# Performance work log

Measured on AMD Instinct MI355X. Metric: run time of the kernel, lower is better.

## Reference

```python
import jax, jax.numpy as jnp
import numpy as np

EPS = 1e-5
DELTA = 0.2
VIS_LAM = 1.0


def setup_inputs() -> dict:
    key = jax.random.key(0)
    k1, k2, k3 = jax.random.split(key, 3)
    Na, Ns, Nb, Ne, D = 16, 32, 100, 12, 512
    vis_feats = jax.random.normal(k1, (Na * Ns * Nb, D), dtype=jnp.float32)
    word_feats = jax.random.normal(k2, (Na * Ne, D), dtype=jnp.float32)
    entities_length = jax.random.randint(k3, (Na,), 0, Ne).astype(jnp.int64)
    return {"vis_feats": vis_feats, "word_feats": word_feats,
            "entities_length": entities_length, "Nb": Nb}


def reference(vis_feats, word_feats, entities_length, Nb):
    Na = entities_length.shape[0]
    Ne = word_feats.shape[0] // Na
    Ns = vis_feats.shape[0] // (Na * Nb)
    D = vis_feats.shape[1]
    ent = entities_length

    div_vec = jnp.where(ent == 0, 1, ent).astype(vis_feats.dtype)      # (Na,)
    # pad mask: entity slot e is padding for action a if e >= ent[a]
    col_mask = jnp.arange(Ne)[None, :] >= ent[:, None]                 # (Na, Ne)

    # masked similarity: (Na*Ns*Nb, Na*Ne)
    S_ = vis_feats @ word_feats.T
    S_ = jnp.where(col_mask.reshape(-1)[None, :], 0.0, S_)

    # --- train-only visual consistency loss ---
    S_vt = S_.reshape(Na, Ns, Nb, Na, Ne)
    # diagonal over the two action axes: S_vis[i] = S_vt[i,:,:,i,:]
    S_vis = S_vt[jnp.arange(Na), :, :, jnp.arange(Na), :]              # (Na, Ns, Nb, Ne)
    S_vis_ng = jax.lax.stop_gradient(S_vis)                            # torch.no_grad block
    sim_scr = S_vis_ng.max(axis=2)                                     # (Na, Ns, Ne)
    maxind = jnp.argmax(S_vis_ng, axis=2)                              # (Na, Ns, Ne)
    smin = sim_scr.min(axis=1, keepdims=True)
    smax = sim_scr.max(axis=1, keepdims=True)
    sim_scr = ((sim_scr - smin) / (smax - smin + EPS))[..., None]      # (Na, Ns, Ne, 1)

    # NOTE: original code indexes vis_feats with the raw box index (< Nb);
    # reproduced faithfully.
    vcls = vis_feats[maxind.reshape(-1)].reshape(Na, Ns, Ne, D)
    vcls = vcls / (jnp.linalg.norm(vcls, axis=3, keepdims=True) + EPS)
    vcls = vcls * sim_scr
    v1 = vcls.transpose(0, 2, 1, 3)                                    # (Na, Ne, Ns, D)
    vis_mat = 1.0 - jnp.einsum('aesd,aetd->aest', v1, v1)              # (Na, Ne, Ns, Ns)
    eye = jnp.eye(Ns, dtype=bool)
    mvis = col_mask[:, :, None, None] | eye[None, None, :, :]
    vis_mat = jnp.where(mvis, 0.0, vis_mat)
    dem = jnp.count_nonzero(vis_mat).astype(vis_mat.dtype)
    vis_loss = vis_mat.sum() / dem

    # --- margin loss over frame-level scores ---
    S = S_.reshape(Na * Ns, Nb, Na * Ne).max(axis=1).reshape(Na, Ns, Na * Ne)
    Smin = S.min(axis=1, keepdims=True)
    Smax = S.max(axis=1, keepdims=True)
    S = S * ((S - Smin) / (Smax - Smin + EPS))
    Sf = S.reshape(Na, Ns, Na, Ne).sum(-1) / div_vec                   # (Na, Ns, Na)
    Sf_diag = Sf[jnp.arange(Na), :, jnp.arange(Na)]                    # (Na, Ns)
    term1 = jax.nn.relu(Sf - Sf_diag.T[None, :, :] + DELTA).mean(0).T  # (Na, Ns)
    term2 = jax.nn.relu(Sf - Sf_diag[:, :, None] + DELTA).mean(2)      # (Na, Ns)
    frame_score = term1 + term2
    margin_loss = (frame_score.mean() + VIS_LAM * vis_loss) * 10.0

    S_sim = S_.reshape(Na * Ns, Nb, Na * Ne)
    D_sim = S_sim.max(axis=1)
    D_ind = jnp.argmax(S_sim, axis=1)
    return (D_ind, D_sim, margin_loss)
```

## Files before the change

kernel.cpp:

```cpp
#include <hip/hip_runtime.h>
#include <math.h>

#define NA 16
#define NS 32
#define NB 100
#define NE 12
#define DD 512
#define NQ (NA*NS)
#define NC (NA*NE)
#define OUT_SIM_OFF (NQ*NC)
#define EPSF 1e-5f
#define DELTAF 0.2f
#define EPS_R 0.15f

#define WS_B_FOFF 12288

typedef _Float16 f16x8 __attribute__((ext_vector_type(8)));
typedef float f32x4 __attribute__((ext_vector_type(4)));

__global__ __launch_bounds__(64) void k0_conv(
    const float* __restrict__ word, float* __restrict__ ws)
{
    const int kcc = blockIdx.x / 12;
    const int nt  = blockIdx.x - kcc*12;
    const int l   = threadIdx.x;
    if (blockIdx.x == 0 && l < 2) ws[l] = 0.f;

    const int col = nt*16 + (l & 15);
    const int k   = kcc*32 + (l >> 4)*8;
    const float* src = word + (size_t)col*DD + k;
    float4 v0 = *(const float4*)(src);
    float4 v1 = *(const float4*)(src + 4);
    f16x8 hv;
    hv[0]=(_Float16)v0.x; hv[1]=(_Float16)v0.y; hv[2]=(_Float16)v0.z; hv[3]=(_Float16)v0.w;
    hv[4]=(_Float16)v1.x; hv[5]=(_Float16)v1.y; hv[6]=(_Float16)v1.z; hv[7]=(_Float16)v1.w;
    unsigned short* wsB = (unsigned short*)(ws + WS_B_FOFF);
    *(f16x8*)&wsB[(size_t)kcc*6144 + nt*512 + l*8] = hv;
}

__global__ __launch_bounds__(512, 4) void k1_mfma(
    const float* __restrict__ vis, const float* __restrict__ word,
    const unsigned short* __restrict__ wsB,
    const int* __restrict__ ent, float* __restrict__ out)
{
    __shared__ __align__(16) char pool[40960];
    unsigned short* Abuf = (unsigned short*)pool;
    unsigned short* Bbuf = (unsigned short*)(pool + 16384);
    float* part_v = (float*)pool;
    int*   part_i = (int*)(pool + 1536);
    float* colmax = (float*)(pool + 3072);
    int*   cnts   = (int*)(pool + 3840);
    int*   cand   = (int*)(pool + 4608);
    int*   flist  = (int*)(pool + 5376);
    int*   nflag  = (int*)(pool + 6144);

    const int t    = threadIdx.x;
    const int lane = t & 63;
    const int wid  = t >> 6;
    const int wm   = wid >> 2;
    const int wn   = wid & 3;
    const int q    = blockIdx.x;
    const float* visq = vis + (size_t)q * NB * DD;

    f32x4 acc[4][3];
    #pragma unroll
    for (int mi = 0; mi < 4; mi++)
        #pragma unroll
        for (int ni = 0; ni < 3; ni++) acc[mi][ni] = (f32x4)0.f;

    #define A_LOAD(av0, av1, kb)                                               \
        {   int l_ = t & 63;                                                   \
            int row = ((t >> 6) << 4) + (l_ & 15);                             \
            av0 = make_float4(0.f,0.f,0.f,0.f);                                \
            av1 = make_float4(0.f,0.f,0.f,0.f);                                \
            if (row < NB) {                                                    \
                const float* p_ = visq + (size_t)row*DD + (kb) + ((l_>>4)<<3); \
                av0 = *(const float4*)p_;                                      \
                av1 = *(const float4*)(p_ + 4); } }
    #define A_STORE(av0, av1, pn)                                              \
        {   f16x8 hv;                                                          \
            hv[0]=(_Float16)av0.x; hv[1]=(_Float16)av0.y;                      \
            hv[2]=(_Float16)av0.z; hv[3]=(_Float16)av0.w;                      \
            hv[4]=(_Float16)av1.x; hv[5]=(_Float16)av1.y;                      \
            hv[6]=(_Float16)av1.z; hv[7]=(_Float16)av1.w;                      \
            *(f16x8*)&Abuf[(pn)*4096 + t*8] = hv; }
    #define B_STAGE(kcn, pn)                                                   \
        {   const unsigned short* bsrc = wsB + (size_t)(kcn)*6144;             \
            unsigned short* bdst = Bbuf + (pn)*6144;                           \
            __builtin_amdgcn_global_load_lds(                                  \
                (const void*)(bsrc + ((size_t)(wid*64 + lane))*8),             \
                (void*)(bdst + (wid*64)*8), 16, 0, 0);                         \
            if (wid < 4)                                                       \
                __builtin_amdgcn_global_load_lds(                              \
                    (const void*)(bsrc + ((size_t)(512 + wid*64 + lane))*8),   \
                    (void*)(bdst + (512 + wid*64)*8), 16, 0, 0); }

    {
        B_STAGE(0, 0);
        float4 a0, a1;
        A_LOAD(a0, a1, 0);
        A_STORE(a0, a1, 0);
    }
    __syncthreads();

    for (int kc = 0; kc < 16; ++kc) {
        const int p = kc & 1;
        float4 a0, a1;
        if (kc < 15) {
            A_LOAD(a0, a1, (kc+1)*32);
            B_STAGE(kc+1, p^1);
        }
        {
            const unsigned short* Bp = Bbuf + p*6144;
            const unsigned short* Ap = Abuf + p*4096;
            f16x8 bf[3];
            #pragma unroll
            for (int ni = 0; ni < 3; ni++)
                bf[ni] = *((const f16x8*)&Bp[(wn*3 + ni)*512 + lane*8]);
            #pragma unroll
            for (int mi = 0; mi < 4; mi++) {
                f16x8 af = *((const f16x8*)&Ap[(wm*4 + mi)*512 + lane*8]);
                #pragma unroll
                for (int ni = 0; ni < 3; ni++)
                    acc[mi][ni] = __builtin_amdgcn_mfma_f32_16x16x32_f16(af, bf[ni], acc[mi][ni], 0, 0, 0);
            }
        }
        if (kc < 15) { A_STORE(a0, a1, (p^1)); }
        __syncthreads();
    }

    #pragma unroll
    for (int ni = 0; ni < 3; ni++) {
        float bv = -INFINITY; int bg = 1000;
        #pragma unroll
        for (int mi = 0; mi < 4; mi++)
            #pragma unroll
            for (int r = 0; r < 4; r++) {
                int g = wm*64 + mi*16 + ((lane>>4)<<2) + r;
                float v = acc[mi][ni][r];
                if (g < NB && (v > bv || (v == bv && g < bg))) { bv = v; bg = g; }
            }
        #pragma unroll
        for (int off = 16; off <= 32; off <<= 1) {
            float ov = __shfl_xor(bv, off);
            int   og = __shfl_xor(bg, off);
            if (ov > bv || (ov == bv && og < bg)) { bv = ov; bg = og; }
        }
        if (lane < 16) {
            int col = wn*48 + ni*16 + lane;
            part_v[wm*NC + col] = bv; part_i[wm*NC + col] = bg;
        }
    }
    if (t < NC) { cnts[t] = 0; cand[t] = 0; }
    if (t == 0) *nflag = 0;
    __syncthreads();

    float fbv = 0.f; int fbg = 0; bool fmask = true;
    if (t < NC) {
        fbv = part_v[t]; fbg = part_i[t];
        float v1 = part_v[NC + t]; int g1 = part_i[NC + t];
        if (v1 > fbv || (v1 == fbv && g1 < fbg)) { fbv = v1; fbg = g1; }
        int a2 = t / NE, e = t - a2*NE;
        fmask = (e >= ent[a2]);
        colmax[t] = fmask ? INFINITY : fbv;
    }
    __syncthreads();

    #pragma unroll
    for (int ni = 0; ni < 3; ni++) {
        int col = wn*48 + ni*16 + (lane & 15);
        float cm = colmax[col] - EPS_R;
        #pragma unroll
        for (int mi = 0; mi < 4; mi++)
            #pragma unroll
            for (int r = 0; r < 4; r++) {
                int g = wm*64 + mi*16 + ((lane>>4)<<2) + r;
                float v = acc[mi][ni][r];
                if (g < NB && v >= cm) {
                    int s = atomicAdd(&cnts[col], 1);
                    if (s < 3) atomicOr(&cand[col], (g + 1) << (8*s));
                }
            }
    }
    __syncthreads();

    if (t < NC) {
        if (fmask) {
            out[(size_t)q*NC + t] = 0.f;
            out[OUT_SIM_OFF + (size_t)q*NC + t] = 0.f;
        } else if (cnts[t] <= 1) {
            out[(size_t)q*NC + t] = (float)fbg;
            out[OUT_SIM_OFF + (size_t)q*NC + t] = fbv;
        } else {
            int idx = atomicAdd(nflag, 1);
            flist[idx] = t;
        }
    }
    __syncthreads();

    const int nf = *nflag;
    for (int f = wid; f < nf; f += 8) {
        int col = flist[f];
        int cnt = cnts[col];
        const float* wc = word + (size_t)col*DD;
        float bv; int bg;
        if (cnt <= 3) {
            int grp = lane >> 4, li = lane & 15;
            int cpk = cand[col];
            int myrow = (grp < cnt) ? (((cpk >> (8*grp)) & 255) - 1) : -1;
            float d = 0.f;
            if (myrow >= 0) {
                const float* vr = visq + (size_t)myrow*DD + li*32;
                const float* wb = wc + li*32;
                #pragma unroll
                for (int m = 0; m < 8; ++m) {
                    float4 a = *(const float4*)(vr + m*4);
                    float4 b = *(const float4*)(wb + m*4);
                    d = fmaf(a.x, b.x, d); d = fmaf(a.y, b.y, d);
                    d = fmaf(a.z, b.z, d); d = fmaf(a.w, b.w, d);
                }
            }
            #pragma unroll
            for (int off = 1; off <= 8; off <<= 1) d += __shfl_xor(d, off);
            float v0 = __shfl(d, 0), v1 = __shfl(d, 16), v2 = __shfl(d, 32);
            int r0 = ( cpk        & 255) - 1;
            int r1 = ((cpk >> 8)  & 255) - 1;
            int r2 = ((cpk >> 16) & 255) - 1;
            bv = v0; bg = r0;
            if (cnt >= 2 && (v1 > bv || (v1 == bv && r1 < bg))) { bv = v1; bg = r1; }
            if (cnt >= 3 && (v2 > bv || (v2 == bv && r2 < bg))) { bv = v2; bg = r2; }
        } else {
            float mbv = -INFINITY; int mbg = 1000;
            for (int r = lane; r < NB; r += 64) {
                float d = 0.f;
                const float* vr = visq + (size_t)r*DD;
                for (int m = 0; m < DD/4; ++m) {
                    float4 a = *(const float4*)(vr + m*4);
                    float4 b = *(const float4*)(wc + m*4);
                    d = fmaf(a.x, b.x, d); d = fmaf(a.y, b.y, d);
                    d = fmaf(a.z, b.z, d); d = fmaf(a.w, b.w, d);
                }
                if (d > mbv || (d == mbv && r < mbg)) { mbv = d; mbg = r; }
            }
            bv = mbv; bg = mbg;
            #pragma unroll
            for (int off = 32; off >= 1; off >>= 1) {
                float ov = __shfl_xor(bv, off); int og = __shfl_xor(bg, off);
                if (ov > bv || (ov == bv && og < bg)) { bv = ov; bg = og; }
            }
        }
        if (lane == 0) {
            out[(size_t)q*NC + col] = (float)bg;
            out[OUT_SIM_OFF + (size_t)q*NC + col] = bv;
        }
    }
}

__global__ __launch_bounds__(256) void k2_vis(
    const float* __restrict__ vis, const int* __restrict__ ent,
    const float* __restrict__ out_ro, float* __restrict__ ws)
{
    const int a = blockIdx.x / NE;
    const int e = blockIdx.x - a*NE;
    if (e >= ent[a]) return;

    __shared__ float VT[DD*36];
    __shared__ float simv[NS];
    __shared__ int   indv[NS];
    __shared__ float scl[NS];
    __shared__ float wsum[4], wcnt[4];
    const int t = threadIdx.x;

    if (t < NS) {
        int q = a*NS + t;
        simv[t] = out_ro[OUT_SIM_OFF + (size_t)q*NC + a*NE + e];
        indv[t] = (int)out_ro[(size_t)q*NC + a*NE + e];
    }
    __syncthreads();
    if (t < NS) {
        float v = simv[t];
        float mn = v, mx = v;
        #pragma unroll
        for (int off = 16; off >= 1; off >>= 1) {
            mn = fminf(mn, __shfl_xor(mn, off));
            mx = fmaxf(mx, __shfl_xor(mx, off));
        }
        simv[t] = (v - mn) / (mx - mn + EPSF);
    }
    __syncthreads();

    const int g = t >> 3, j = t & 7;
    const float* src = vis + (size_t)indv[g]*DD;
    float ss = 0.f;
    #pragma unroll
    for (int i = 0; i < 16; i++) {
        int k4 = j + 8*i;
        float4 v = *(const float4*)(src + k4*4);
        ss = fmaf(v.x,v.x, fmaf(v.y,v.y, fmaf(v.z,v.z, fmaf(v.w,v.w, ss))));
        int k = k4*4;
        VT[(k+0)*36 + g] = v.x;
        VT[(k+1)*36 + g] = v.y;
        VT[(k+2)*36 + g] = v.z;
        VT[(k+3)*36 + g] = v.w;
    }
    #pragma unroll
    for (int off = 4; off >= 1; off >>= 1) ss += __shfl_xor(ss, off);
    if (j == 0) scl[g] = simv[g] / (sqrtf(ss) + EPSF);
    __syncthreads();

    const int s = t >> 3, tq = t & 7;
    float g0=0.f, g1=0.f, g2=0.f, g3=0.f;
    for (int k = 0; k < DD; k++) {
        float vs = VT[k*36 + s];
        float4 vt = *(const float4*)&VT[k*36 + tq*4];
        g0 = fmaf(vs, vt.x, g0);
        g1 = fmaf(vs, vt.y, g1);
        g2 = fmaf(vs, vt.z, g2);
        g3 = fmaf(vs, vt.w, g3);
    }
    float lsum = 0.f, lcnt = 0.f;
    float sc_s = scl[s];
    float gv[4] = {g0, g1, g2, g3};
    #pragma unroll
    for (int jj = 0; jj < 4; jj++) {
        int tt = tq*4 + jj;
        if (tt != s) {
            float val = 1.f - sc_s * scl[tt] * gv[jj];
            lsum += val;
            if (val != 0.f) lcnt += 1.f;
        }
    }
    #pragma unroll
    for (int off = 32; off >= 1; off >>= 1) {
        lsum += __shfl_xor(lsum, off);
        lcnt += __shfl_xor(lcnt, off);
    }
    const int wid = t >> 6, lane = t & 63;
    if (lane == 0) { wsum[wid] = lsum; wcnt[wid] = lcnt; }
    __syncthreads();
    if (t == 0) {
        atomicAdd(&ws[0], wsum[0]+wsum[1]+wsum[2]+wsum[3]);
        atomicAdd(&ws[1], wcnt[0]+wcnt[1]+wcnt[2]+wcnt[3]);
    }
}

__global__ __launch_bounds__(256) void k3_margin(
    const float* __restrict__ out_ro, const int* __restrict__ ent,
    float* __restrict__ ws)
{
    const int a = blockIdx.x;
    __shared__ float Ss[NS][NC];
    __shared__ float Smn[NC], Smx[NC];
    const int t = threadIdx.x;
    for (int e2 = t; e2 < NS*NC; e2 += 256) {
        int s = e2 / NC, c = e2 - (e2/NC)*NC;
        Ss[s][c] = out_ro[OUT_SIM_OFF + (size_t)(a*NS + s)*NC + c];
    }
    __syncthreads();
    if (t < NC) {
        float mn = INFINITY, mx = -INFINITY;
        #pragma unroll
        for (int s = 0; s < NS; s++) {
            float v = Ss[s][t];
            mn = fminf(mn, v); mx = fmaxf(mx, v);
        }
        Smn[t] = mn; Smx[t] = mx;
    }
    __syncthreads();
    for (int p = t; p < NS*NA; p += 256) {
        int s = p >> 4, b = p & 15;
        int eb = ent[b];
        float dv = (eb == 0) ? 1.f : (float)eb;
        float sum = 0.f;
        #pragma unroll
        for (int e2 = 0; e2 < NE; e2++) {
            int c = b*NE + e2;
            float S = Ss[s][c];
            float r = (S - Smn[c]) / (Smx[c] - Smn[c] + EPSF);
            sum += S * r;
        }
        ws[2 + a*(NS*NA) + s*NA + b] = sum / dv;
    }
}

__global__ __launch_bounds__(256) void k4_final(
    const float* __restrict__ ws_ro, float* __restrict__ out)
{
    __shared__ float Sf[NA][NS][NA];
    __shared__ float dg[NA][NS];
    __shared__ float wred[4];
    const int t = threadIdx.x;
    for (int e2 = t; e2 < NA*NS*NA; e2 += 256)
        ((float*)Sf)[e2] = ws_ro[2 + e2];
    __syncthreads();
    for (int p = t; p < NA*NS; p += 256) {
        int aa = p >> 5, s = p & 31;
        dg[aa][s] = Sf[aa][s][aa];
    }
    __syncthreads();
    float fsum = 0.f;
    for (int p = t; p < NA*NS; p += 256) {
        int i = p >> 5, s = p & 31;
        float d = dg[i][s];
        float t1 = 0.f, t2 = 0.f;
        #pragma unroll
        for (int x = 0; x < NA; x++) {
            t1 += fmaxf(Sf[x][s][i] - d + DELTAF, 0.f);
            t2 += fmaxf(Sf[i][s][x] - d + DELTAF, 0.f);
        }
        fsum += (t1 + t2) * (1.f/16.f);
    }
    #pragma unroll
    for (int off = 32; off >= 1; off >>= 1) fsum += __shfl_xor(fsum, off);
    const int wid = t >> 6, lane = t & 63;
    if (lane == 0) wred[wid] = fsum;
    __syncthreads();
    if (t == 0) {
        float frame_mean = (wred[0]+wred[1]+wred[2]+wred[3]) / 512.f;
        float vis_loss = ws_ro[0] / ws_ro[1];
        out[2*OUT_SIM_OFF] = (frame_mean + 1.0f * vis_loss) * 10.f;
    }
}

extern "C" void kernel_launch(void* const* d_in, const int* in_sizes, int n_in,
                              void* d_out, int out_size, void* d_ws, size_t ws_size,
                              hipStream_t stream)
{
    (void)in_sizes; (void)n_in; (void)out_size; (void)ws_size;
    const float* vis  = (const float*)d_in[0];
    const float* word = (const float*)d_in[1];
    const int*   ent  = (const int*)d_in[2];
    float* out = (float*)d_out;
    float* ws  = (float*)d_ws;
    const unsigned short* wsB = (const unsigned short*)(ws + WS_B_FOFF);

    k0_conv<<<192, 64, 0, stream>>>(word, ws);
    k1_mfma<<<NQ, 512, 0, stream>>>(vis, word, wsB, ent, out);
    k2_vis<<<NA*NE, 256, 0, stream>>>(vis, ent, out, ws);
    k3_margin<<<NA, 256, 0, stream>>>(out, ent, ws);
    k4_final<<<1, 256, 0, stream>>>(ws, out);
}
```

Before: 62.69 us.

## Load A fragments directly to registers, dropping the LDS staging buffer

The A operand (visual features) is now loaded by each wave straight from global memory into registers in MFMA fragment layout and converted to f16 in registers, so the LDS A buffer and its stores go away. B is still staged through LDS with global_load_lds, and the loop replaces __syncthreads with manual vmcnt waits, s_barrier and sched_barrier to overlap the next chunk's loads with the current MFMAs. Shared memory drops from 40 KB to 24 KB. In exchange, the 4 waves that share each 64-row A slice (one per wn) each load it, so A global traffic is multiplied by four. Register pressure also rises from holding 8 float4 prefetch registers, and the hand-tuned vmcnt count must match the issue order exactly.

```diff
diff --git a/kernel.cpp b/kernel.cpp
--- a/kernel.cpp
+++ b/kernel.cpp
@@ -43,9 +43,8 @@
     const unsigned short* __restrict__ wsB,
     const int* __restrict__ ent, float* __restrict__ out)
 {
-    __shared__ __align__(16) char pool[40960];
-    unsigned short* Abuf = (unsigned short*)pool;
-    unsigned short* Bbuf = (unsigned short*)(pool + 16384);
+    __shared__ __align__(16) char pool[24576];
+    unsigned short* Bbuf = (unsigned short*)pool;
     float* part_v = (float*)pool;
     int*   part_i = (int*)(pool + 1536);
     float* colmax = (float*)(pool + 3072);
@@ -68,22 +67,25 @@
         #pragma unroll
         for (int ni = 0; ni < 3; ni++) acc[mi][ni] = (f32x4)0.f;
 
-    #define A_LOAD(av0, av1, kb)                                               \
-        {   int l_ = t & 63;                                                   \
-            int row = ((t >> 6) << 4) + (l_ & 15);                             \
-            av0 = make_float4(0.f,0.f,0.f,0.f);                                \
-            av1 = make_float4(0.f,0.f,0.f,0.f);                                \
-            if (row < NB) {                                                    \
-                const float* p_ = visq + (size_t)row*DD + (kb) + ((l_>>4)<<3); \
-                av0 = *(const float4*)p_;                                      \
-                av1 = *(const float4*)(p_ + 4); } }
-    #define A_STORE(av0, av1, pn)                                              \
-        {   f16x8 hv;                                                          \
-            hv[0]=(_Float16)av0.x; hv[1]=(_Float16)av0.y;                      \
-            hv[2]=(_Float16)av0.z; hv[3]=(_Float16)av0.w;                      \
-            hv[4]=(_Float16)av1.x; hv[5]=(_Float16)av1.y;                      \
-            hv[6]=(_Float16)av1.z; hv[7]=(_Float16)av1.w;                      \
-            *(f16x8*)&Abuf[(pn)*4096 + t*8] = hv; }
+    float4 ar0[4], ar1[4];
+
+    #define A_ISSUE(kb)                                                        \
+        _Pragma("unroll")                                                      \
+        for (int mi = 0; mi < 4; mi++) {                                       \
+            int row = wm*64 + mi*16 + (lane & 15);                             \
+            row = row < NB ? row : 0;     \
+            const float* p_ = visq + (size_t)row*DD + (kb) + ((lane>>4)<<3);   \
+            ar0[mi] = *(const float4*)p_;                                      \
+            ar1[mi] = *(const float4*)(p_ + 4);                                \
+        }
+    #define A_CVT(af)                                                          \
+        _Pragma("unroll")                                                      \
+        for (int mi = 0; mi < 4; mi++) {                                       \
+            af[mi][0]=(_Float16)ar0[mi].x; af[mi][1]=(_Float16)ar0[mi].y;      \
+            af[mi][2]=(_Float16)ar0[mi].z; af[mi][3]=(_Float16)ar0[mi].w;      \
+            af[mi][4]=(_Float16)ar1[mi].x; af[mi][5]=(_Float16)ar1[mi].y;      \
+            af[mi][6]=(_Float16)ar1[mi].z; af[mi][7]=(_Float16)ar1[mi].w;      \
+        }
     #define B_STAGE(kcn, pn)                                                   \
         {   const unsigned short* bsrc = wsB + (size_t)(kcn)*6144;             \
             unsigned short* bdst = Bbuf + (pn)*6144;                           \
@@ -95,38 +97,43 @@
                     (const void*)(bsrc + ((size_t)(512 + wid*64 + lane))*8),   \
                     (void*)(bdst + (512 + wid*64)*8), 16, 0, 0); }
 
-    {
-        B_STAGE(0, 0);
-        float4 a0, a1;
-        A_LOAD(a0, a1, 0);
-        A_STORE(a0, a1, 0);
-    }
-    __syncthreads();
+    B_STAGE(0, 0);
+    __builtin_amdgcn_sched_barrier(0);
+    A_ISSUE(0);
+    __builtin_amdgcn_sched_barrier(0);
+    asm volatile("s_waitcnt vmcnt(8)" ::: "memory");
+    __builtin_amdgcn_s_barrier();
+    __builtin_amdgcn_sched_barrier(0);
 
     for (int kc = 0; kc < 16; ++kc) {
         const int p = kc & 1;
-        float4 a0, a1;
         if (kc < 15) {
-            A_LOAD(a0, a1, (kc+1)*32);
             B_STAGE(kc+1, p^1);
+            __builtin_amdgcn_sched_barrier(0);
+        }
+        f16x8 af[4];
+        A_CVT(af);
+        if (kc < 15) {
+            A_ISSUE((kc+1)*32);
+            __builtin_amdgcn_sched_barrier(0);
         }
         {
             const unsigned short* Bp = Bbuf + p*6144;
-            const unsigned short* Ap = Abuf + p*4096;
             f16x8 bf[3];
             #pragma unroll
             for (int ni = 0; ni < 3; ni++)
                 bf[ni] = *((const f16x8*)&Bp[(wn*3 + ni)*512 + lane*8]);
             #pragma unroll
-            for (int mi = 0; mi < 4; mi++) {
-                f16x8 af = *((const f16x8*)&Ap[(wm*4 + mi)*512 + lane*8]);
+            for (int mi = 0; mi < 4; mi++)
                 #pragma unroll
                 for (int ni = 0; ni < 3; ni++)
-                    acc[mi][ni] = __builtin_amdgcn_mfma_f32_16x16x32_f16(af, bf[ni], acc[mi][ni], 0, 0, 0);
-            }
-        }
-        if (kc < 15) { A_STORE(a0, a1, (p^1)); }
-        __syncthreads();
+                    acc[mi][ni] = __builtin_amdgcn_mfma_f32_16x16x32_f16(af[mi], bf[ni], acc[mi][ni], 0, 0, 0);
+        }
+        if (kc < 15) {
+            asm volatile("s_waitcnt vmcnt(8)" ::: "memory");
+            __builtin_amdgcn_s_barrier();
+            __builtin_amdgcn_sched_barrier(0);
+        }
     }
 
     #pragma unroll
```

After: 179.0 us. 186% more time.

## Double K-chunk size in MFMA GEMM pipeline and merge vis/margin kernels into one launch

Applied to the files above, without the earlier changes.

The main MFMA kernel now stages 64-wide K chunks, so it runs 8 iterations instead of 16. Each iteration loads twice as much A and B data, which halves the barrier count and deepens each prefetch. The word-matrix conversion writes a matching interleaved layout. Separately, the visual-consistency and margin kernels become a single launch that branches on block index, removing one kernel launch. The cost is doubled LDS in the GEMM kernel (80KB), which may cut blocks per CU, plus more registers for the prefetched A data.

```diff
diff --git a/kernel.cpp b/kernel.cpp
--- a/kernel.cpp
+++ b/kernel.cpp
@@ -35,7 +35,8 @@
     hv[0]=(_Float16)v0.x; hv[1]=(_Float16)v0.y; hv[2]=(_Float16)v0.z; hv[3]=(_Float16)v0.w;
     hv[4]=(_Float16)v1.x; hv[5]=(_Float16)v1.y; hv[6]=(_Float16)v1.z; hv[7]=(_Float16)v1.w;
     unsigned short* wsB = (unsigned short*)(ws + WS_B_FOFF);
-    *(f16x8*)&wsB[(size_t)kcc*6144 + nt*512 + l*8] = hv;
+    const int kc2 = kcc >> 1, ks = kcc & 1;
+    *(f16x8*)&wsB[(size_t)(((kc2*12 + nt)*2 + ks)*512) + l*8] = hv;
 }
 
 __global__ __launch_bounds__(512, 4) void k1_mfma(
@@ -43,9 +44,9 @@
     const unsigned short* __restrict__ wsB,
     const int* __restrict__ ent, float* __restrict__ out)
 {
-    __shared__ __align__(16) char pool[40960];
+    __shared__ __align__(16) char pool[81920];
     unsigned short* Abuf = (unsigned short*)pool;
-    unsigned short* Bbuf = (unsigned short*)(pool + 16384);
+    unsigned short* Bbuf = (unsigned short*)(pool + 32768);
     float* part_v = (float*)pool;
     int*   part_i = (int*)(pool + 1536);
     float* colmax = (float*)(pool + 3072);
@@ -68,64 +69,73 @@
         #pragma unroll
         for (int ni = 0; ni < 3; ni++) acc[mi][ni] = (f32x4)0.f;
 
-    #define A_LOAD(av0, av1, kb)                                               \
+    float4 ar[4];
+
+    #define A_LOAD(kb)                                                         \
         {   int l_ = t & 63;                                                   \
             int row = ((t >> 6) << 4) + (l_ & 15);                             \
-            av0 = make_float4(0.f,0.f,0.f,0.f);                                \
-            av1 = make_float4(0.f,0.f,0.f,0.f);                                \
+            ar[0] = make_float4(0.f,0.f,0.f,0.f); ar[1] = ar[0];               \
+            ar[2] = ar[0]; ar[3] = ar[0];                                      \
             if (row < NB) {                                                    \
                 const float* p_ = visq + (size_t)row*DD + (kb) + ((l_>>4)<<3); \
-                av0 = *(const float4*)p_;                                      \
-                av1 = *(const float4*)(p_ + 4); } }
-    #define A_STORE(av0, av1, pn)                                              \
-        {   f16x8 hv;                                                          \
-            hv[0]=(_Float16)av0.x; hv[1]=(_Float16)av0.y;                      \
-            hv[2]=(_Float16)av0.z; hv[3]=(_Float16)av0.w;                      \
-            hv[4]=(_Float16)av1.x; hv[5]=(_Float16)av1.y;                      \
-            hv[6]=(_Float16)av1.z; hv[7]=(_Float16)av1.w;                      \
-            *(f16x8*)&Abuf[(pn)*4096 + t*8] = hv; }
+                ar[0] = *(const float4*)p_;                                    \
+                ar[1] = *(const float4*)(p_ + 4);                              \
+                ar[2] = *(const float4*)(p_ + 32);                             \
+                ar[3] = *(const float4*)(p_ + 36); } }
+    #define A_STORE(pn)                                                       \
+        {   int mt_ = t >> 6;                                                 \
+            f16x8 h0, h1;                                                     \
+            h0[0]=(_Float16)ar[0].x; h0[1]=(_Float16)ar[0].y;                 \
+            h0[2]=(_Float16)ar[0].z; h0[3]=(_Float16)ar[0].w;                 \
+            h0[4]=(_Float16)ar[1].x; h0[5]=(_Float16)ar[1].y;                 \
+            h0[6]=(_Float16)ar[1].z; h0[7]=(_Float16)ar[1].w;                 \
+            h1[0]=(_Float16)ar[2].x; h1[1]=(_Float16)ar[2].y;                 \
+            h1[2]=(_Float16)ar[2].z; h1[3]=(_Float16)ar[2].w;                 \
+            h1[4]=(_Float16)ar[3].x; h1[5]=(_Float16)ar[3].y;                 \
+            h1[6]=(_Float16)ar[3].z; h1[7]=(_Float16)ar[3].w;                 \
+            *(f16x8*)&Abuf[(pn)*8192 + (mt_*2+0)*512 + (t&63)*8] = h0;        \
+            *(f16x8*)&Abuf[(pn)*8192 + (mt_*2+1)*512 + (t&63)*8] = h1; }
     #define B_STAGE(kcn, pn)                                                   \
-        {   const unsigned short* bsrc = wsB + (size_t)(kcn)*6144;             \
-            unsigned short* bdst = Bbuf + (pn)*6144;                           \
-            __builtin_amdgcn_global_load_lds(                                  \
-                (const void*)(bsrc + ((size_t)(wid*64 + lane))*8),             \
-                (void*)(bdst + (wid*64)*8), 16, 0, 0);                         \
-            if (wid < 4)                                                       \
+        {   const unsigned short* bsrc = wsB + (size_t)(kcn)*12288;            \
+            unsigned short* bdst = Bbuf + (pn)*12288;                          \
+            _Pragma("unroll")                                                  \
+            for (int i = 0; i < 3; i++)                                        \
                 __builtin_amdgcn_global_load_lds(                              \
-                    (const void*)(bsrc + ((size_t)(512 + wid*64 + lane))*8),   \
-                    (void*)(bdst + (512 + wid*64)*8), 16, 0, 0); }
+                    (const void*)(bsrc + ((size_t)(i*512 + wid*64 + lane))*8), \
+                    (void*)(bdst + (i*512 + wid*64)*8), 16, 0, 0); }
 
     {
         B_STAGE(0, 0);
-        float4 a0, a1;
-        A_LOAD(a0, a1, 0);
-        A_STORE(a0, a1, 0);
-    }
-    __syncthreads();
-
-    for (int kc = 0; kc < 16; ++kc) {
+        A_LOAD(0);
+        A_STORE(0);
+    }
+    __syncthreads();
+
+    for (int kc = 0; kc < 8; ++kc) {
         const int p = kc & 1;
-        float4 a0, a1;
-        if (kc < 15) {
-            A_LOAD(a0, a1, (kc+1)*32);
+        if (kc < 7) {
+            A_LOAD((kc+1)*64);
             B_STAGE(kc+1, p^1);
         }
         {
-            const unsigned short* Bp = Bbuf + p*6144;
-            const unsigned short* Ap = Abuf + p*4096;
-            f16x8 bf[3];
-            #pragma unroll
-            for (int ni = 0; ni < 3; ni++)
-                bf[ni] = *((const f16x8*)&Bp[(wn*3 + ni)*512 + lane*8]);
-            #pragma unroll
-            for (int mi = 0; mi < 4; mi++) {
-                f16x8 af = *((const f16x8*)&Ap[(wm*4 + mi)*512 + lane*8]);
+            const unsigned short* Bp = Bbuf + p*12288;
+            const unsigned short* Ap = Abuf + p*8192;
+            #pragma unroll
+            for (int ks = 0; ks < 2; ks++) {
+                f16x8 bf[3];
                 #pragma unroll
                 for (int ni = 0; ni < 3; ni++)
-                    acc[mi][ni] = __builtin_amdgcn_mfma_f32_16x16x32_f16(af, bf[ni], acc[mi][ni], 0, 0, 0);
-            }
-        }
-        if (kc < 15) { A_STORE(a0, a1, (p^1)); }
+                    bf[ni] = *((const f16x8*)&Bp[((wn*3 + ni)*2 + ks)*512 + lane*8]);
+                #pragma unroll
+                for (int mi = 0; mi < 4; mi++) {
+                    f16x8 af = *((const f16x8*)&Ap[((wm*4 + mi)*2 + ks)*512 + lane*8]);
+                    #pragma unroll
+                    for (int ni = 0; ni < 3; ni++)
+                        acc[mi][ni] = __builtin_amdgcn_mfma_f32_16x16x32_f16(af, bf[ni], acc[mi][ni], 0, 0, 0);
+                }
+            }
+        }
+        if (kc < 7) { A_STORE(p^1); }
         __syncthreads();
     }
 
@@ -256,130 +266,131 @@
     }
 }
 
-__global__ __launch_bounds__(256) void k2_vis(
+__global__ __launch_bounds__(256) void k23_fused(
     const float* __restrict__ vis, const int* __restrict__ ent,
     const float* __restrict__ out_ro, float* __restrict__ ws)
 {
-    const int a = blockIdx.x / NE;
-    const int e = blockIdx.x - a*NE;
-    if (e >= ent[a]) return;
-
-    __shared__ float VT[DD*36];
-    __shared__ float simv[NS];
-    __shared__ int   indv[NS];
-    __shared__ float scl[NS];
-    __shared__ float wsum[4], wcnt[4];
+    __shared__ __align__(16) char pool[74240];
     const int t = threadIdx.x;
 
-    if (t < NS) {
-        int q = a*NS + t;
-        simv[t] = out_ro[OUT_SIM_OFF + (size_t)q*NC + a*NE + e];
-        indv[t] = (int)out_ro[(size_t)q*NC + a*NE + e];
-    }
-    __syncthreads();
-    if (t < NS) {
-        float v = simv[t];
-        float mn = v, mx = v;
-        #pragma unroll
-        for (int off = 16; off >= 1; off >>= 1) {
-            mn = fminf(mn, __shfl_xor(mn, off));
-            mx = fmaxf(mx, __shfl_xor(mx, off));
-        }
-        simv[t] = (v - mn) / (mx - mn + EPSF);
-    }
-    __syncthreads();
-
-    const int g = t >> 3, j = t & 7;
-    const float* src = vis + (size_t)indv[g]*DD;
-    float ss = 0.f;
-    #pragma unroll
-    for (int i = 0; i < 16; i++) {
-        int k4 = j + 8*i;
-        float4 v = *(const float4*)(src + k4*4);
-        ss = fmaf(v.x,v.x, fmaf(v.y,v.y, fmaf(v.z,v.z, fmaf(v.w,v.w, ss))));
-        int k = k4*4;
-        VT[(k+0)*36 + g] = v.x;
-        VT[(k+1)*36 + g] = v.y;
-        VT[(k+2)*36 + g] = v.z;
-        VT[(k+3)*36 + g] = v.w;
-    }
-    #pragma unroll
-    for (int off = 4; off >= 1; off >>= 1) ss += __shfl_xor(ss, off);
-    if (j == 0) scl[g] = simv[g] / (sqrtf(ss) + EPSF);
-    __syncthreads();
-
-    const int s = t >> 3, tq = t & 7;
-    float g0=0.f, g1=0.f, g2=0.f, g3=0.f;
-    for (int k = 0; k < DD; k++) {
-        float vs = VT[k*36 + s];
-        float4 vt = *(const float4*)&VT[k*36 + tq*4];
-        g0 = fmaf(vs, vt.x, g0);
-        g1 = fmaf(vs, vt.y, g1);
-        g2 = fmaf(vs, vt.z, g2);
-        g3 = fmaf(vs, vt.w, g3);
-    }
-    float lsum = 0.f, lcnt = 0.f;
-    float sc_s = scl[s];
-    float gv[4] = {g0, g1, g2, g3};
-    #pragma unroll
-    for (int jj = 0; jj < 4; jj++) {
-        int tt = tq*4 + jj;
-        if (tt != s) {
-            float val = 1.f - sc_s * scl[tt] * gv[jj];
-            lsum += val;
-            if (val != 0.f) lcnt += 1.f;
-        }
-    }
-    #pragma unroll
-    for (int off = 32; off >= 1; off >>= 1) {
-        lsum += __shfl_xor(lsum, off);
-        lcnt += __shfl_xor(lcnt, off);
-    }
-    const int wid = t >> 6, lane = t & 63;
-    if (lane == 0) { wsum[wid] = lsum; wcnt[wid] = lcnt; }
-    __syncthreads();
-    if (t == 0) {
-        atomicAdd(&ws[0], wsum[0]+wsum[1]+wsum[2]+wsum[3]);
-        atomicAdd(&ws[1], wcnt[0]+wcnt[1]+wcnt[2]+wcnt[3]);
-    }
-}
-
-__global__ __launch_bounds__(256) void k3_margin(
-    const float* __restrict__ out_ro, const int* __restrict__ ent,
-    float* __restrict__ ws)
-{
-    const int a = blockIdx.x;
-    __shared__ float Ss[NS][NC];
-    __shared__ float Smn[NC], Smx[NC];
-    const int t = threadIdx.x;
-    for (int e2 = t; e2 < NS*NC; e2 += 256) {
-        int s = e2 / NC, c = e2 - (e2/NC)*NC;
-        Ss[s][c] = out_ro[OUT_SIM_OFF + (size_t)(a*NS + s)*NC + c];
-    }
-    __syncthreads();
-    if (t < NC) {
-        float mn = INFINITY, mx = -INFINITY;
-        #pragma unroll
-        for (int s = 0; s < NS; s++) {
-            float v = Ss[s][t];
-            mn = fminf(mn, v); mx = fmaxf(mx, v);
-        }
-        Smn[t] = mn; Smx[t] = mx;
-    }
-    __syncthreads();
-    for (int p = t; p < NS*NA; p += 256) {
-        int s = p >> 4, b = p & 15;
-        int eb = ent[b];
-        float dv = (eb == 0) ? 1.f : (float)eb;
-        float sum = 0.f;
-        #pragma unroll
-        for (int e2 = 0; e2 < NE; e2++) {
-            int c = b*NE + e2;
-            float S = Ss[s][c];
-            float r = (S - Smn[c]) / (Smx[c] - Smn[c] + EPSF);
-            sum += S * r;
-        }
-        ws[2 + a*(NS*NA) + s*NA + b] = sum / dv;
+    if (blockIdx.x < 192) {
+        const int a = blockIdx.x / NE;
+        const int e = blockIdx.x - a*NE;
+        if (e >= ent[a]) return;
+
+        float* VT   = (float*)pool;
+        float* simv = (float*)(pool + 73728);
+        int*   indv = (int*)(pool + 73856);
+        float* scl  = (float*)(pool + 73984);
+        float* wsum = (float*)(pool + 74112);
+        float* wcnt = (float*)(pool + 74128);
+
+        if (t < NS) {
+            int q = a*NS + t;
+            simv[t] = out_ro[OUT_SIM_OFF + (size_t)q*NC + a*NE + e];
+            indv[t] = (int)out_ro[(size_t)q*NC + a*NE + e];
+        }
+        __syncthreads();
+        if (t < NS) {
+            float v = simv[t];
+            float mn = v, mx = v;
+            #pragma unroll
+            for (int off = 16; off >= 1; off >>= 1) {
+                mn = fminf(mn, __shfl_xor(mn, off));
+                mx = fmaxf(mx, __shfl_xor(mx, off));
+            }
+            simv[t] = (v - mn) / (mx - mn + EPSF);
+        }
+        __syncthreads();
+
+        const int g = t >> 3, j = t & 7;
+        const float* src = vis + (size_t)indv[g]*DD;
+        float ss = 0.f;
+        #pragma unroll
+        for (int i = 0; i < 16; i++) {
+            int k4 = j + 8*i;
+            float4 v = *(const float4*)(src + k4*4);
+            ss = fmaf(v.x,v.x, fmaf(v.y,v.y, fmaf(v.z,v.z, fmaf(v.w,v.w, ss))));
+            int k = k4*4;
+            VT[(k+0)*36 + g] = v.x;
+            VT[(k+1)*36 + g] = v.y;
+            VT[(k+2)*36 + g] = v.z;
+            VT[(k+3)*36 + g] = v.w;
+        }
+        #pragma unroll
+        for (int off = 4; off >= 1; off >>= 1) ss += __shfl_xor(ss, off);
+        if (j == 0) scl[g] = simv[g] / (sqrtf(ss) + EPSF);
+        __syncthreads();
+
+        const int s = t >> 3, tq = t & 7;
+        float g0=0.f, g1=0.f, g2=0.f, g3=0.f;
+        for (int k = 0; k < DD; k++) {
+            float vs = VT[k*36 + s];
+            float4 vt = *(const float4*)&VT[k*36 + tq*4];
+            g0 = fmaf(vs, vt.x, g0);
+            g1 = fmaf(vs, vt.y, g1);
+            g2 = fmaf(vs, vt.z, g2);
+            g3 = fmaf(vs, vt.w, g3);
+        }
+        float lsum = 0.f, lcnt = 0.f;
+        float sc_s = scl[s];
+        float gv[4] = {g0, g1, g2, g3};
+        #pragma unroll
+        for (int jj = 0; jj < 4; jj++) {
+            int tt = tq*4 + jj;
+            if (tt != s) {
+                float val = 1.f - sc_s * scl[tt] * gv[jj];
+                lsum += val;
+                if (val != 0.f) lcnt += 1.f;
+            }
+        }
+        #pragma unroll
+        for (int off = 32; off >= 1; off >>= 1) {
+            lsum += __shfl_xor(lsum, off);
+            lcnt += __shfl_xor(lcnt, off);
+        }
+        const int wid = t >> 6, lane = t & 63;
+        if (lane == 0) { wsum[wid] = lsum; wcnt[wid] = lcnt; }
+        __syncthreads();
+        if (t == 0) {
+            atomicAdd(&ws[0], wsum[0]+wsum[1]+wsum[2]+wsum[3]);
+            atomicAdd(&ws[1], wcnt[0]+wcnt[1]+wcnt[2]+wcnt[3]);
+        }
+    } else {
+        const int a = blockIdx.x - 192;
+        float* Ss  = (float*)pool;
+        float* Smn = (float*)(pool + 24576);
+        float* Smx = (float*)(pool + 25344);
+
+        for (int e2 = t; e2 < NS*NC; e2 += 256) {
+            int s = e2 / NC, c = e2 - (e2/NC)*NC;
+            Ss[s*NC + c] = out_ro[OUT_SIM_OFF + (size_t)(a*NS + s)*NC + c];
+        }
+        __syncthreads();
+        if (t < NC) {
+            float mn = INFINITY, mx = -INFINITY;
+            #pragma unroll
+            for (int s = 0; s < NS; s++) {
+                float v = Ss[s*NC + t];
+                mn = fminf(mn, v); mx = fmaxf(mx, v);
+            }
+            Smn[t] = mn; Smx[t] = mx;
+        }
+        __syncthreads();
+        for (int p = t; p < NS*NA; p += 256) {
+            int s = p >> 4, b = p & 15;
+            int eb = ent[b];
+            float dv = (eb == 0) ? 1.f : (float)eb;
+            float sum = 0.f;
+            #pragma unroll
+            for (int e2 = 0; e2 < NE; e2++) {
+                int c = b*NE + e2;
+                float S = Ss[s*NC + c];
+                float r = (S - Smn[c]) / (Smx[c] - Smn[c] + EPSF);
+                sum += S * r;
+            }
+            ws[2 + a*(NS*NA) + s*NA + b] = sum / dv;
+        }
     }
 }
 
@@ -436,7 +447,6 @@
 
     k0_conv<<<192, 64, 0, stream>>>(word, ws);
     k1_mfma<<<NQ, 512, 0, stream>>>(vis, word, wsB, ent, out);
-    k2_vis<<<NA*NE, 256, 0, stream>>>(vis, ent, out, ws);
-    k3_margin<<<NA, 256, 0, stream>>>(out, ent, ws);
+    k23_fused<<<208, 256, 0, stream>>>(vis, ent, out, ws);
     k4_final<<<1, 256, 0, stream>>>(ws, out);
 }
```

Measured after the change: 56.89 us, median of 3. 9.3% less time.
